# Kernel tuning notes

Hardware: AMD Instinct MI355X
Metric: run time of the kernel (lower is better)

Reference implementation:

```python
import jax, jax.numpy as jnp
import numpy as np

B, L, D, H, NS = 8, 1024, 64, 16, 3
DH = D // H          # head dim = 4 (scale = sqrt(4) = 2, matching K_.size(-1)**0.5)
DFF = 4 * D          # 256
EPS = 1e-5


def _bn(x_bld, gamma, beta):
    # BatchNorm1d in training mode on (B, C, L): normalize per-channel over (B, L)
    mean = jnp.mean(x_bld, axis=(0, 1))          # [D]
    var = jnp.mean((x_bld - mean) ** 2, axis=(0, 1))  # biased variance, as torch uses
    return gamma * (x_bld - mean) / jnp.sqrt(var + EPS) + beta


def setup_inputs() -> dict:
    key = jax.random.key(0)
    ks = jax.random.split(key, 12)
    s = 0.05
    inp = {
        "x": jax.random.normal(ks[0], (B, L, D), dtype=jnp.float32),
        # W_embed: Conv1d(64,64,k=1) == linear over channels
        "W_embed": jax.random.normal(ks[1], (D, D), dtype=jnp.float32) * s,
        "b_embed": jnp.zeros((D,), dtype=jnp.float32),
        "g0": jnp.ones((D,), dtype=jnp.float32),
        "be0": jnp.zeros((D,), dtype=jnp.float32),
        # shared attention weights (reused every stack)
        "Wq": jax.random.normal(ks[2], (D, D), dtype=jnp.float32) * s,
        "bq": jnp.zeros((D,), dtype=jnp.float32),
        "Wk": jax.random.normal(ks[3], (D, D), dtype=jnp.float32) * s,
        "bk": jnp.zeros((D,), dtype=jnp.float32),
        "Wv": jax.random.normal(ks[4], (D, D), dtype=jnp.float32) * s,
        "bv": jnp.zeros((D,), dtype=jnp.float32),
        "g_attn": jnp.ones((D,), dtype=jnp.float32),
        "be_attn": jnp.zeros((D,), dtype=jnp.float32),
        # shared feedforward (1x1 convs == channel linears)
        "W1": jax.random.normal(ks[5], (DFF, D), dtype=jnp.float32) * s,
        "b1": jnp.zeros((DFF,), dtype=jnp.float32),
        "W2": jax.random.normal(ks[6], (D, DFF), dtype=jnp.float32) * s,
        "b2": jnp.zeros((D,), dtype=jnp.float32),
        "g_ff": jnp.ones((D,), dtype=jnp.float32),
        "be_ff": jnp.zeros((D,), dtype=jnp.float32),
    }
    return inp


def reference(x, W_embed, b_embed, g0, be0, Wq, bq, Wk, bk, Wv, bv,
              g_attn, be_attn, W1, b1, W2, b2, g_ff, be_ff):
    # input embedding (1x1 conv) + batchnorm
    enc = x @ W_embed.T + b_embed              # [B, L, D]
    enc = _bn(enc, g0, be0)

    for _ in range(NS):  # num_stacks, SAME weights each stack (as in source)
        # --- multi-head attention (ReLU-activated QKV projections) ---
        Q = jax.nn.relu(enc @ Wq.T + bq)        # [B, L, D]
        K = jax.nn.relu(enc @ Wk.T + bk)
        V = jax.nn.relu(enc @ Wv.T + bv)
        q = Q.reshape(B, L, H, DH)
        k = K.reshape(B, L, H, DH)
        v = V.reshape(B, L, H, DH)
        scores = jnp.einsum('blhd,bmhd->bhlm', q, k) / jnp.sqrt(jnp.float32(DH))
        A = jax.nn.softmax(scores, axis=-1)     # [B, H, L, L]
        o = jnp.einsum('bhlm,bmhd->blhd', A, v).reshape(B, L, D)
        o = o + enc                             # residual
        enc = _bn(o, g_attn, be_attn)

        # --- feedforward: conv1d(k=1) -> ReLU -> conv1d(k=1) -> ReLU, residual, BN ---
        h = jax.nn.relu(enc @ W1.T + b1)        # [B, L, 4D]
        h = jax.nn.relu(h @ W2.T + b2)          # [B, L, D]
        h = h + enc                             # residual
        enc = _bn(h, g_ff, be_ff)
    return enc
```

## Files before the change

### kernel.cpp

```cpp
#include <hip/hip_runtime.h>
#include <math.h>

static constexpr int B_ = 8, L_ = 1024, D_ = 64, H_ = 16, DH_ = 4, DFF_ = 256;
static constexpr int M_ = B_ * L_;
static constexpr float EPS_ = 1e-5f;
static constexpr float INV_N_ = 1.0f / (float)M_;
static constexpr int PSTR_ = 512;

typedef _Float16 half4_ __attribute__((ext_vector_type(4)));
typedef __fp16   fp16x2 __attribute__((ext_vector_type(2)));
typedef float    f32x4  __attribute__((ext_vector_type(4)));

__global__ __launch_bounds__(256) void embed_kernel(
    const float* __restrict__ x, const float* __restrict__ W_embed,
    const float* __restrict__ wq, const float* __restrict__ wk,
    const float* __restrict__ wv, const float* __restrict__ w1,
    const float* __restrict__ w2, const float* __restrict__ bias,
    float* __restrict__ C, float* __restrict__ outParts,
    _Float16* __restrict__ wdst)
{
    const int t = threadIdx.x;
    {
        int base = (blockIdx.x * 256 + t) * 2;
        #pragma unroll
        for (int i = 0; i < 2; ++i) {
            int e = base + i;
            if (e < 45056) {
                float v;
                if      (e <  4096) v = wq[e];
                else if (e <  8192) v = wk[e - 4096];
                else if (e < 12288) v = wv[e - 8192];
                else if (e < 28672) v = w1[e - 12288];
                else                v = w2[e - 28672];
                wdst[e] = (_Float16)v;
            }
        }
    }

    __shared__ half4_ Alds[64][17];
    __shared__ half4_ Wlds[64][17];
    __shared__ float  wstats[4][128];
    const int m0 = blockIdx.x * 64;

    #pragma unroll
    for (int i = 0; i < 4; ++i) {
        int l = i * 256 + t;
        int row = l >> 4, c4 = l & 15;
        float4 av = *(const float4*)&x[(size_t)(m0 + row) * 64 + c4 * 4];
        Alds[row][c4] = half4_{(_Float16)av.x, (_Float16)av.y,
                               (_Float16)av.z, (_Float16)av.w};
        float4 wv4 = *(const float4*)&W_embed[(size_t)row * 64 + c4 * 4];
        Wlds[row][c4] = half4_{(_Float16)wv4.x, (_Float16)wv4.y,
                               (_Float16)wv4.z, (_Float16)wv4.w};
    }
    __syncthreads();

    const int lane = t & 63, w = t >> 6, g = lane >> 4, ml = lane & 15;

    f32x4 acc[4] = {};
    #pragma unroll
    for (int kci = 0; kci < 4; ++kci) {
        half4_ af = Alds[w * 16 + ml][kci * 4 + g];
        #pragma unroll
        for (int nt = 0; nt < 4; ++nt) {
            half4_ wf = Wlds[nt * 16 + ml][kci * 4 + g];
            acc[nt] = __builtin_amdgcn_mfma_f32_16x16x16f16(wf, af, acc[nt], 0, 0, 0);
        }
    }

    const int m = m0 + w * 16 + ml;
    float sv[4][4], qv[4][4];
    #pragma unroll
    for (int nt = 0; nt < 4; ++nt) {
        const int nc = nt * 16 + 4 * g;
        float4 bv4 = *(const float4*)&bias[nc];
        float r0 = acc[nt][0] + bv4.x, r1 = acc[nt][1] + bv4.y;
        float r2 = acc[nt][2] + bv4.z, r3 = acc[nt][3] + bv4.w;
        float4 o4 = { r0, r1, r2, r3 };
        *(float4*)&C[(size_t)m * 64 + nc] = o4;
        sv[nt][0] = r0; sv[nt][1] = r1; sv[nt][2] = r2; sv[nt][3] = r3;
        qv[nt][0] = r0 * r0; qv[nt][1] = r1 * r1;
        qv[nt][2] = r2 * r2; qv[nt][3] = r3 * r3;
    }

    #pragma unroll
    for (int d = 1; d <= 8; d <<= 1)
        #pragma unroll
        for (int nt = 0; nt < 4; ++nt)
            #pragma unroll
            for (int r = 0; r < 4; ++r) {
                sv[nt][r] += __shfl_xor(sv[nt][r], d);
                qv[nt][r] += __shfl_xor(qv[nt][r], d);
            }
    if (ml == 0) {
        #pragma unroll
        for (int nt = 0; nt < 4; ++nt)
            #pragma unroll
            for (int r = 0; r < 4; ++r) {
                int ch = nt * 16 + 4 * g + r;
                wstats[w][ch]      = sv[nt][r];
                wstats[w][64 + ch] = qv[nt][r];
            }
    }
    __syncthreads();
    if (t < 128) {
        float a = wstats[0][t] + wstats[1][t] + wstats[2][t] + wstats[3][t];
        outParts[(size_t)t * PSTR_ + blockIdx.x] = a;
    }
}

template<int NPB>
__global__ __launch_bounds__(256) void qkv_kernel(
    const float* __restrict__ tmpA,
    const _Float16* __restrict__ wqh, const float* __restrict__ bq,
    const _Float16* __restrict__ wkh, const float* __restrict__ bk,
    const _Float16* __restrict__ wvh, const float* __restrict__ bv,
    _Float16* __restrict__ qh, _Float16* __restrict__ kh, _Float16* __restrict__ vh,
    const float* __restrict__ partsIn,
    const float* __restrict__ gg, const float* __restrict__ bb)
{
    __shared__ half4_ Alds[64][17];
    __shared__ half4_ Wlds[64][17];
    __shared__ float  raw[128];
    __shared__ float  bnsc[64], bnsh[64];
    const int t    = threadIdx.x;
    const int m0   = blockIdx.x * 64;
    const int mode = blockIdx.y;

    const _Float16* W = (mode == 0) ? wqh : (mode == 1) ? wkh : wvh;
    const float* bias = (mode == 0) ? bq  : (mode == 1) ? bk  : bv;
    const float  sc2  = (mode == 0) ? 0.5f * 1.44269504088896340736f : 1.f;

    if (t < 128) {
        const float* pr = partsIn + (size_t)t * PSTR_;
        float a = 0.f;
        #pragma unroll
        for (int j = 0; j < NPB; j += 4) {
            float4 v4 = *(const float4*)&pr[j];
            a += v4.x + v4.y + v4.z + v4.w;
        }
        raw[t] = a;
    }
    __syncthreads();
    if (t < 64) {
        float mean = raw[t] * INV_N_;
        float ex2  = raw[64 + t] * INV_N_;
        float rs   = rsqrtf(ex2 - mean * mean + EPS_);
        float s2   = gg[t] * rs;
        bnsc[t] = s2;
        bnsh[t] = bb[t] - mean * s2;
    }
    __syncthreads();

    #pragma unroll
    for (int i = 0; i < 4; ++i) {
        int l = i * 256 + t;
        int row = l >> 4, c4 = l & 15;
        float4 av = *(const float4*)&tmpA[(size_t)(m0 + row) * 64 + c4 * 4];
        int c = c4 * 4;
        av.x = fmaf(av.x, bnsc[c + 0], bnsh[c + 0]);
        av.y = fmaf(av.y, bnsc[c + 1], bnsh[c + 1]);
        av.z = fmaf(av.z, bnsc[c + 2], bnsh[c + 2]);
        av.w = fmaf(av.w, bnsc[c + 3], bnsh[c + 3]);
        Alds[row][c4] = half4_{(_Float16)av.x, (_Float16)av.y,
                               (_Float16)av.z, (_Float16)av.w};
        Wlds[row][c4] = *(const half4_*)&W[(size_t)row * 64 + c4 * 4];
    }
    __syncthreads();

    const int lane = t & 63, w = t >> 6, g = lane >> 4, ml = lane & 15;

    f32x4 acc[4] = {};
    #pragma unroll
    for (int kci = 0; kci < 4; ++kci) {
        half4_ af = Alds[w * 16 + ml][kci * 4 + g];
        #pragma unroll
        for (int nt = 0; nt < 4; ++nt) {
            half4_ wf = Wlds[nt * 16 + ml][kci * 4 + g];
            acc[nt] = __builtin_amdgcn_mfma_f32_16x16x16f16(wf, af, acc[nt], 0, 0, 0);
        }
    }

    const int m    = m0 + w * 16 + ml;
    const int bidx = m >> 10, row = m & 1023;
    #pragma unroll
    for (int nt = 0; nt < 4; ++nt) {
        const int nc = nt * 16 + 4 * g;
        const int h  = nc >> 2;
        float4 bv4 = *(const float4*)&bias[nc];
        float r0 = fmaxf(acc[nt][0] + bv4.x, 0.f) * sc2;
        float r1 = fmaxf(acc[nt][1] + bv4.y, 0.f) * sc2;
        float r2 = fmaxf(acc[nt][2] + bv4.z, 0.f) * sc2;
        float r3 = fmaxf(acc[nt][3] + bv4.w, 0.f) * sc2;
        if (mode == 2) {
            size_t base = ((size_t)(bidx * 16 + h) * 4) * 1024 + row;
            vh[base + 0]    = (_Float16)r0;
            vh[base + 1024] = (_Float16)r1;
            vh[base + 2048] = (_Float16)r2;
            vh[base + 3072] = (_Float16)r3;
        } else {
            _Float16* Cq = (mode == 0) ? qh : kh;
            half4_ hs = { (_Float16)r0, (_Float16)r1, (_Float16)r2, (_Float16)r3 };
            *(half4_*)&Cq[((size_t)(bidx * 16 + h) * 1024 + row) * 4] = hs;
        }
    }
}

__global__ __launch_bounds__(256) void ffused_kernel(
    const float* __restrict__ tmpB, const _Float16* __restrict__ w1h,
    const float* __restrict__ b1, const _Float16* __restrict__ w2h,
    const float* __restrict__ b2, float* __restrict__ tmpA,
    const float* __restrict__ partsB,
    const float* __restrict__ gg, const float* __restrict__ bb,
    float* __restrict__ outParts)
{
    __shared__ half4_   Alds[16][17];
    __shared__ _Float16 H[16][264];
    __shared__ float    raw[128];
    __shared__ float    bnsc[64], bnsh[64];
    const int t  = threadIdx.x;
    const int m0 = blockIdx.x * 16;

    if (t < 128) {
        const float* pr = partsB + (size_t)t * PSTR_;
        float a = 0.f;
        #pragma unroll
        for (int j = 0; j < 64; j += 4) {
            float4 v4 = *(const float4*)&pr[j];
            a += v4.x + v4.y + v4.z + v4.w;
        }
        raw[t] = a;
    }
    __syncthreads();
    if (t < 64) {
        float mean = raw[t] * INV_N_;
        float ex2  = raw[64 + t] * INV_N_;
        float rs   = rsqrtf(ex2 - mean * mean + EPS_);
        float s2   = gg[t] * rs;
        bnsc[t] = s2;
        bnsh[t] = bb[t] - mean * s2;
    }
    __syncthreads();

    {
        int row = t >> 4, c4 = t & 15;
        float4 av = *(const float4*)&tmpB[(size_t)(m0 + row) * 64 + c4 * 4];
        int c = c4 * 4;
        av.x = fmaf(av.x, bnsc[c + 0], bnsh[c + 0]);
        av.y = fmaf(av.y, bnsc[c + 1], bnsh[c + 1]);
        av.z = fmaf(av.z, bnsc[c + 2], bnsh[c + 2]);
        av.w = fmaf(av.w, bnsc[c + 3], bnsh[c + 3]);
        Alds[row][c4] = half4_{(_Float16)av.x, (_Float16)av.y,
                               (_Float16)av.z, (_Float16)av.w};
    }
    __syncthreads();

    const int lane = t & 63, w = t >> 6, g = lane >> 4, ml = lane & 15;

    f32x4 acc1[4] = {};
    #pragma unroll
    for (int kci = 0; kci < 4; ++kci) {
        half4_ af = Alds[ml][kci * 4 + g];
        #pragma unroll
        for (int ntl = 0; ntl < 4; ++ntl) {
            int nt = w * 4 + ntl;
            half4_ wf = *(const half4_*)&w1h[(size_t)(nt * 16 + ml) * 64 + kci * 16 + 4 * g];
            acc1[ntl] = __builtin_amdgcn_mfma_f32_16x16x16f16(wf, af, acc1[ntl], 0, 0, 0);
        }
    }
    #pragma unroll
    for (int ntl = 0; ntl < 4; ++ntl) {
        int nt = w * 4 + ntl;
        float4 b1v = *(const float4*)&b1[nt * 16 + 4 * g];
        half4_ hv = { (_Float16)fmaxf(acc1[ntl][0] + b1v.x, 0.f),
                      (_Float16)fmaxf(acc1[ntl][1] + b1v.y, 0.f),
                      (_Float16)fmaxf(acc1[ntl][2] + b1v.z, 0.f),
                      (_Float16)fmaxf(acc1[ntl][3] + b1v.w, 0.f) };
        *(half4_*)&H[ml][nt * 16 + 4 * g] = hv;
    }
    __syncthreads();

    f32x4 acc2 = {};
    #pragma unroll
    for (int kci2 = 0; kci2 < 16; ++kci2) {
        half4_ af2 = *(const half4_*)&H[ml][kci2 * 16 + 4 * g];
        half4_ wf2 = *(const half4_*)&w2h[(size_t)(w * 16 + ml) * 256 + kci2 * 16 + 4 * g];
        acc2 = __builtin_amdgcn_mfma_f32_16x16x16f16(wf2, af2, acc2, 0, 0, 0);
    }

    const int m  = m0 + ml;
    const int nc = w * 16 + 4 * g;
    float4 b2v = *(const float4*)&b2[nc];
    half4_ rr  = Alds[ml][w * 4 + g];
    float r0 = fmaxf(acc2[0] + b2v.x, 0.f) + (float)rr[0];
    float r1 = fmaxf(acc2[1] + b2v.y, 0.f) + (float)rr[1];
    float r2 = fmaxf(acc2[2] + b2v.z, 0.f) + (float)rr[2];
    float r3 = fmaxf(acc2[3] + b2v.w, 0.f) + (float)rr[3];
    float4 o4 = { r0, r1, r2, r3 };
    *(float4*)&tmpA[(size_t)m * 64 + nc] = o4;

    float sv[4] = { r0, r1, r2, r3 };
    float qv[4] = { r0 * r0, r1 * r1, r2 * r2, r3 * r3 };
    #pragma unroll
    for (int d = 1; d <= 8; d <<= 1)
        #pragma unroll
        for (int r = 0; r < 4; ++r) {
            sv[r] += __shfl_xor(sv[r], d);
            qv[r] += __shfl_xor(qv[r], d);
        }
    if (ml == 0) {
        #pragma unroll
        for (int r = 0; r < 4; ++r) {
            outParts[(size_t)(nc + r) * PSTR_ + blockIdx.x]      = sv[r];
            outParts[(size_t)(64 + nc + r) * PSTR_ + blockIdx.x] = qv[r];
        }
    }
}

template<int NPB>
__global__ __launch_bounds__(256) void attn_kernel(
    const _Float16* __restrict__ q, const _Float16* __restrict__ k,
    const _Float16* __restrict__ v, const float* __restrict__ encRaw,
    float* __restrict__ out, const float* __restrict__ partsIn,
    const float* __restrict__ gPrev, const float* __restrict__ bPrev,
    float* __restrict__ partsOut)
{
    __shared__ uint2 klds[1024];
    __shared__ uint2 vlds[1024];
    __shared__ float raw8[8], rsc[4], rsh[4];
    __shared__ float wred[4][8];

    const int bid = blockIdx.x;
    const int qc  = bid & 7;
    const int h   = (bid >> 3) & 15;
    const int b   = bid >> 7;
    const int t   = threadIdx.x;

    if (t < 8) {
        const int row = (t >> 2) * 64 + 4 * h + (t & 3);
        const float* pr = partsIn + (size_t)row * PSTR_;
        float a = 0.f;
        #pragma unroll
        for (int j = 0; j < NPB; j += 4) {
            float4 v4 = *(const float4*)&pr[j];
            a += v4.x + v4.y + v4.z + v4.w;
        }
        raw8[t] = a;
    }
    if (t < 4) {
        float mean = raw8[t] * INV_N_;
        float ex2  = raw8[4 + t] * INV_N_;
        float rs   = rsqrtf(ex2 - mean * mean + EPS_);
        float s2   = gPrev[4 * h + t] * rs;
        rsc[t] = s2;
        rsh[t] = bPrev[4 * h + t] - mean * s2;
    }

    const size_t baseqk = (size_t)(b * 16 + h) * 4096;

    #pragma unroll
    for (int i = 0; i < 4; ++i) {
        int key = i * 256 + t;
        klds[key] = *(const uint2*)&k[baseqk + (size_t)key * 4];
        int e = (t >> 2) * 16 + (t & 3) * 4 + i;
        vlds[e] = *(const uint2*)&v[baseqk + (size_t)i * 1024 + t * 4];
    }
    __syncthreads();

    const int lane = t & 63;
    const int wv2  = t >> 6;
    const int ln16 = lane & 15;
    const int g16  = lane >> 4;
    const int q0   = qc * 128 + wv2 * 32;

    half4_ qf0 = { 0, 0, 0, 0 }, qf1 = { 0, 0, 0, 0 };
    if (lane < 16) {
        qf0 = __builtin_bit_cast(half4_,
              *(const uint2*)&q[baseqk + (size_t)(q0 + ln16) * 4]);
        qf1 = __builtin_bit_cast(half4_,
              *(const uint2*)&q[baseqk + (size_t)(q0 + 16 + ln16) * 4]);
    }

    const half4_ ones = { (_Float16)1.f, (_Float16)1.f, (_Float16)1.f, (_Float16)1.f };
    const f32x4  fz   = { 0.f, 0.f, 0.f, 0.f };
    f32x4 o0 = fz, o1 = fz;

    #pragma unroll 4
    for (int c = 0; c < 64; ++c) {
        half4_ ka = __builtin_bit_cast(half4_, klds[c * 16 + ln16]);
        half4_ va = __builtin_bit_cast(half4_, vlds[c * 16 + g16 * 4 + (ln16 & 3)]);
        if (ln16 == 4) va = ones;

        f32x4 s0 = __builtin_amdgcn_mfma_f32_16x16x16f16(ka, qf0, fz, 0, 0, 0);
        f32x4 s1 = __builtin_amdgcn_mfma_f32_16x16x16f16(ka, qf1, fz, 0, 0, 0);

        float e00 = __builtin_amdgcn_exp2f(s0[0]);
        float e01 = __builtin_amdgcn_exp2f(s0[1]);
        float e02 = __builtin_amdgcn_exp2f(s0[2]);
        float e03 = __builtin_amdgcn_exp2f(s0[3]);
        float e10 = __builtin_amdgcn_exp2f(s1[0]);
        float e11 = __builtin_amdgcn_exp2f(s1[1]);
        float e12 = __builtin_amdgcn_exp2f(s1[2]);
        float e13 = __builtin_amdgcn_exp2f(s1[3]);

        fp16x2 a0 = __builtin_amdgcn_cvt_pkrtz(e00, e01);
        fp16x2 b0 = __builtin_amdgcn_cvt_pkrtz(e02, e03);
        fp16x2 a1 = __builtin_amdgcn_cvt_pkrtz(e10, e11);
        fp16x2 b1 = __builtin_amdgcn_cvt_pkrtz(e12, e13);
        half4_ p0 = __builtin_bit_cast(half4_, __builtin_shufflevector(a0, b0, 0, 1, 2, 3));
        half4_ p1 = __builtin_bit_cast(half4_, __builtin_shufflevector(a1, b1, 0, 1, 2, 3));

        o0 = __builtin_amdgcn_mfma_f32_16x16x16f16(va, p0, o0, 0, 0, 0);
        o1 = __builtin_amdgcn_mfma_f32_16x16x16f16(va, p1, o1, 0, 0, 0);
    }

    float ls0 = __shfl(o0[0], 16 + ln16);
    float ls1 = __shfl(o1[0], 16 + ln16);

    float4 r0v = { 0.f, 0.f, 0.f, 0.f }, r1v = r0v;
    if (lane < 16) {
        {
            const size_t gi = (size_t)(b * L_ + q0 + ln16) * D_ + h * DH_;
            const float inv = 1.0f / ls0;
            const float4 e4 = *(const float4*)&encRaw[gi];
            r0v.x = fmaf(o0[0], inv, fmaf(e4.x, rsc[0], rsh[0]));
            r0v.y = fmaf(o0[1], inv, fmaf(e4.y, rsc[1], rsh[1]));
            r0v.z = fmaf(o0[2], inv, fmaf(e4.z, rsc[2], rsh[2]));
            r0v.w = fmaf(o0[3], inv, fmaf(e4.w, rsc[3], rsh[3]));
            *(float4*)&out[gi] = r0v;
        }
        {
            const size_t gi = (size_t)(b * L_ + q0 + 16 + ln16) * D_ + h * DH_;
            const float inv = 1.0f / ls1;
            const float4 e4 = *(const float4*)&encRaw[gi];
            r1v.x = fmaf(o1[0], inv, fmaf(e4.x, rsc[0], rsh[0]));
            r1v.y = fmaf(o1[1], inv, fmaf(e4.y, rsc[1], rsh[1]));
            r1v.z = fmaf(o1[2], inv, fmaf(e4.z, rsc[2], rsh[2]));
            r1v.w = fmaf(o1[3], inv, fmaf(e4.w, rsc[3], rsh[3]));
            *(float4*)&out[gi] = r1v;
        }
    }

    float s4[4] = { r0v.x + r1v.x, r0v.y + r1v.y, r0v.z + r1v.z, r0v.w + r1v.w };
    float q4[4] = { r0v.x*r0v.x + r1v.x*r1v.x, r0v.y*r0v.y + r1v.y*r1v.y,
                    r0v.z*r0v.z + r1v.z*r1v.z, r0v.w*r0v.w + r1v.w*r1v.w };
    #pragma unroll
    for (int d2 = 1; d2 <= 8; d2 <<= 1) {
        #pragma unroll
        for (int j = 0; j < 4; ++j) {
            s4[j] += __shfl_xor(s4[j], d2);
            q4[j] += __shfl_xor(q4[j], d2);
        }
    }
    if (lane == 0) {
        #pragma unroll
        for (int j = 0; j < 4; ++j) { wred[wv2][j] = s4[j]; wred[wv2][4 + j] = q4[j]; }
    }
    __syncthreads();
    if (t < 8) {
        float a = wred[0][t] + wred[1][t] + wred[2][t] + wred[3][t];
        const int row = (t >> 2) * 64 + 4 * h + (t & 3);
        partsOut[(size_t)row * PSTR_ + (b * 8 + qc)] = a;
    }
}

__global__ __launch_bounds__(256) void bn_apply_kernel(
    const float* __restrict__ x, const float* __restrict__ parts,
    const float* __restrict__ gamma, const float* __restrict__ beta,
    float* __restrict__ y)
{
    __shared__ float fstats[128];
    const int t = threadIdx.x;
    if (t < 128) {
        const float* pr = parts + (size_t)t * PSTR_;
        float a = 0.f;
        #pragma unroll
        for (int j = 0; j < 512; j += 4) {
            float4 v4 = *(const float4*)&pr[j];
            a += v4.x + v4.y + v4.z + v4.w;
        }
        fstats[t] = a;
    }
    __syncthreads();

    const int idx = blockIdx.x * 256 + t;
    const int c = (idx & 15) << 2;
    float4 xv = ((const float4*)x)[idx];
    float4 sm = *(const float4*)&fstats[c];
    float4 sq = *(const float4*)&fstats[64 + c];
    float4 g  = *(const float4*)&gamma[c];
    float4 be = *(const float4*)&beta[c];

    float mean[4] = {sm.x * INV_N_, sm.y * INV_N_, sm.z * INV_N_, sm.w * INV_N_};
    float ex2[4]  = {sq.x * INV_N_, sq.y * INV_N_, sq.z * INV_N_, sq.w * INV_N_};
    float xa[4] = {xv.x, xv.y, xv.z, xv.w};
    float ga[4] = {g.x, g.y, g.z, g.w};
    float ba[4] = {be.x, be.y, be.z, be.w};
    float ya[4];
    #pragma unroll
    for (int i = 0; i < 4; ++i) {
        float var = ex2[i] - mean[i] * mean[i];
        float rs = rsqrtf(var + EPS_);
        ya[i] = ga[i] * (xa[i] - mean[i]) * rs + ba[i];
    }
    float4 r = {ya[0], ya[1], ya[2], ya[3]};
    ((float4*)y)[idx] = r;
}

extern "C" void kernel_launch(void* const* d_in, const int* in_sizes, int n_in,
                              void* d_out, int out_size, void* d_ws, size_t ws_size,
                              hipStream_t stream)
{
    const float* x       = (const float*)d_in[0];
    const float* W_embed = (const float*)d_in[1];
    const float* b_embed = (const float*)d_in[2];
    const float* g0      = (const float*)d_in[3];
    const float* be0     = (const float*)d_in[4];
    const float* Wq      = (const float*)d_in[5];
    const float* bq      = (const float*)d_in[6];
    const float* Wk      = (const float*)d_in[7];
    const float* bk      = (const float*)d_in[8];
    const float* Wv      = (const float*)d_in[9];
    const float* bv      = (const float*)d_in[10];
    const float* g_attn  = (const float*)d_in[11];
    const float* be_attn = (const float*)d_in[12];
    const float* W1      = (const float*)d_in[13];
    const float* b1      = (const float*)d_in[14];
    const float* W2      = (const float*)d_in[15];
    const float* b2      = (const float*)d_in[16];
    const float* g_ff    = (const float*)d_in[17];
    const float* be_ff   = (const float*)d_in[18];

    float* ws     = (float*)d_ws;
    float* tmpA   = ws;
    float* tmpB   = ws + 524288;
    float* partsA = ws + 1048576;
    float* partsB = ws + 1114112;
    _Float16* hb  = (_Float16*)(ws + 1179648);
    _Float16* qh  = hb;
    _Float16* kh  = hb + 524288;
    _Float16* vh  = hb + 1048576;
    _Float16* wqh = hb + 1572864;
    _Float16* wkh = wqh + 4096;
    _Float16* wvh = wkh + 4096;
    _Float16* w1h = wvh + 4096;
    _Float16* w2h = w1h + 16384;
    float* out = (float*)d_out;

    const dim3 blk(256);

    embed_kernel<<<128, blk, 0, stream>>>(
        x, W_embed, Wq, Wk, Wv, W1, W2, b_embed, tmpA, partsA, wqh);

    for (int s = 0; s < 3; ++s) {
        const float* gP  = (s == 0) ? g0  : g_ff;
        const float* beP = (s == 0) ? be0 : be_ff;
        if (s == 0) {
            qkv_kernel<128><<<dim3(128, 3), blk, 0, stream>>>(
                tmpA, wqh, bq, wkh, bk, wvh, bv, qh, kh, vh, partsA, gP, beP);
            attn_kernel<128><<<1024, blk, 0, stream>>>(
                qh, kh, vh, tmpA, tmpB, partsA, gP, beP, partsB);
        } else {
            qkv_kernel<512><<<dim3(128, 3), blk, 0, stream>>>(
                tmpA, wqh, bq, wkh, bk, wvh, bv, qh, kh, vh, partsA, gP, beP);
            attn_kernel<512><<<1024, blk, 0, stream>>>(
                qh, kh, vh, tmpA, tmpB, partsA, gP, beP, partsB);
        }
        ffused_kernel<<<512, blk, 0, stream>>>(
            tmpB, w1h, b1, w2h, b2, tmpA, partsB, g_attn, be_attn, partsA);
    }
    bn_apply_kernel<<<512, blk, 0, stream>>>(tmpA, partsA, g_ff, be_ff, out);
}
```

Measured before the change: 192.4 us.

## Merge all stages into one cooperative persistent kernel with grid syncs

Result: faster. 172.4 us (-10.4%).

```diff
diff --git a/kernel.cpp b/kernel.cpp
--- a/kernel.cpp
+++ b/kernel.cpp
@@ -1,57 +1,47 @@
 #include <hip/hip_runtime.h>
+#include <hip/hip_cooperative_groups.h>
 #include <math.h>
+
+namespace cg = cooperative_groups;
 
 static constexpr int B_ = 8, L_ = 1024, D_ = 64, H_ = 16, DH_ = 4, DFF_ = 256;
 static constexpr int M_ = B_ * L_;
 static constexpr float EPS_ = 1e-5f;
 static constexpr float INV_N_ = 1.0f / (float)M_;
-static constexpr int PSTR_ = 512;
+static constexpr int PSTR_ = 256;
+static constexpr unsigned SMEM_ = 32768;
 
 typedef _Float16 half4_ __attribute__((ext_vector_type(4)));
 typedef __fp16   fp16x2 __attribute__((ext_vector_type(2)));
 typedef float    f32x4  __attribute__((ext_vector_type(4)));
 
-__global__ __launch_bounds__(256) void embed_kernel(
-    const float* __restrict__ x, const float* __restrict__ W_embed,
-    const float* __restrict__ wq, const float* __restrict__ wk,
-    const float* __restrict__ wv, const float* __restrict__ w1,
-    const float* __restrict__ w2, const float* __restrict__ bias,
-    float* __restrict__ C, float* __restrict__ outParts,
-    _Float16* __restrict__ wdst)
-{
-    const int t = threadIdx.x;
-    {
-        int base = (blockIdx.x * 256 + t) * 2;
-        #pragma unroll
-        for (int i = 0; i < 2; ++i) {
-            int e = base + i;
-            if (e < 45056) {
-                float v;
-                if      (e <  4096) v = wq[e];
-                else if (e <  8192) v = wk[e - 4096];
-                else if (e < 12288) v = wv[e - 8192];
-                else if (e < 28672) v = w1[e - 12288];
-                else                v = w2[e - 28672];
-                wdst[e] = (_Float16)v;
-            }
-        }
-    }
-
-    __shared__ half4_ Alds[64][17];
-    __shared__ half4_ Wlds[64][17];
-    __shared__ float  wstats[4][128];
-    const int m0 = blockIdx.x * 64;
+struct MParams {
+    const float *x, *W_embed, *b_embed, *g0, *be0;
+    const float *Wq, *bq, *Wk, *bk, *Wv, *bv, *g_attn, *be_attn;
+    const float *W1, *b1, *W2, *b2, *g_ff, *be_ff;
+    float *tmpA, *tmpB, *partsA, *partsB;
+    _Float16 *qh, *kh, *vh, *h1, *wqh, *wkh, *wvh, *w1h, *w2h;
+    float *out;
+};
+
+__device__ __forceinline__ void embed_work(char* sm, int blk, const MParams& p)
+{
+    half4_* Alds  = (half4_*)sm;
+    half4_* Wlds  = (half4_*)(sm + 8704);
+    float*  wstat = (float*)(sm + 17408);
+    const int t  = threadIdx.x;
+    const int m0 = blk * 64;
 
     #pragma unroll
     for (int i = 0; i < 4; ++i) {
         int l = i * 256 + t;
         int row = l >> 4, c4 = l & 15;
-        float4 av = *(const float4*)&x[(size_t)(m0 + row) * 64 + c4 * 4];
-        Alds[row][c4] = half4_{(_Float16)av.x, (_Float16)av.y,
-                               (_Float16)av.z, (_Float16)av.w};
-        float4 wv4 = *(const float4*)&W_embed[(size_t)row * 64 + c4 * 4];
-        Wlds[row][c4] = half4_{(_Float16)wv4.x, (_Float16)wv4.y,
-                               (_Float16)wv4.z, (_Float16)wv4.w};
+        float4 av = *(const float4*)&p.x[(size_t)(m0 + row) * 64 + c4 * 4];
+        Alds[row * 17 + c4] = half4_{(_Float16)av.x, (_Float16)av.y,
+                                     (_Float16)av.z, (_Float16)av.w};
+        float4 wv4 = *(const float4*)&p.W_embed[(size_t)row * 64 + c4 * 4];
+        Wlds[row * 17 + c4] = half4_{(_Float16)wv4.x, (_Float16)wv4.y,
+                                     (_Float16)wv4.z, (_Float16)wv4.w};
     }
     __syncthreads();
 
@@ -60,10 +50,10 @@
     f32x4 acc[4] = {};
     #pragma unroll
     for (int kci = 0; kci < 4; ++kci) {
-        half4_ af = Alds[w * 16 + ml][kci * 4 + g];
+        half4_ af = Alds[(w * 16 + ml) * 17 + kci * 4 + g];
         #pragma unroll
         for (int nt = 0; nt < 4; ++nt) {
-            half4_ wf = Wlds[nt * 16 + ml][kci * 4 + g];
+            half4_ wf = Wlds[(nt * 16 + ml) * 17 + kci * 4 + g];
             acc[nt] = __builtin_amdgcn_mfma_f32_16x16x16f16(wf, af, acc[nt], 0, 0, 0);
         }
     }
@@ -73,11 +63,11 @@
     #pragma unroll
     for (int nt = 0; nt < 4; ++nt) {
         const int nc = nt * 16 + 4 * g;
-        float4 bv4 = *(const float4*)&bias[nc];
+        float4 bv4 = *(const float4*)&p.b_embed[nc];
         float r0 = acc[nt][0] + bv4.x, r1 = acc[nt][1] + bv4.y;
         float r2 = acc[nt][2] + bv4.z, r3 = acc[nt][3] + bv4.w;
         float4 o4 = { r0, r1, r2, r3 };
-        *(float4*)&C[(size_t)m * 64 + nc] = o4;
+        *(float4*)&p.tmpA[(size_t)m * 64 + nc] = o4;
         sv[nt][0] = r0; sv[nt][1] = r1; sv[nt][2] = r2; sv[nt][3] = r3;
         qv[nt][0] = r0 * r0; qv[nt][1] = r1 * r1;
         qv[nt][2] = r2 * r2; qv[nt][3] = r3 * r3;
@@ -98,41 +88,50 @@
             #pragma unroll
             for (int r = 0; r < 4; ++r) {
                 int ch = nt * 16 + 4 * g + r;
-                wstats[w][ch]      = sv[nt][r];
-                wstats[w][64 + ch] = qv[nt][r];
+                wstat[w * 128 + ch]      = sv[nt][r];
+                wstat[w * 128 + 64 + ch] = qv[nt][r];
             }
     }
     __syncthreads();
     if (t < 128) {
-        float a = wstats[0][t] + wstats[1][t] + wstats[2][t] + wstats[3][t];
-        outParts[(size_t)t * PSTR_ + blockIdx.x] = a;
+        float a = wstat[t] + wstat[128 + t] + wstat[256 + t] + wstat[384 + t];
+        p.partsA[(size_t)t * PSTR_ + blk] = a;
+    }
+}
+
+__device__ __forceinline__ void wcvt_work(int blk, int t, const MParams& p)
+{
+    int e = (blk - 128) * 256 + t;
+    if (e < 45056) {
+        float v;
+        if      (e <  4096) v = p.Wq[e];
+        else if (e <  8192) v = p.Wk[e - 4096];
+        else if (e < 12288) v = p.Wv[e - 8192];
+        else if (e < 28672) v = p.W1[e - 12288];
+        else                v = p.W2[e - 28672];
+        p.wqh[e] = (_Float16)v;
     }
 }
 
 template<int NPB>
-__global__ __launch_bounds__(256) void qkv_kernel(
-    const float* __restrict__ tmpA,
-    const _Float16* __restrict__ wqh, const float* __restrict__ bq,
-    const _Float16* __restrict__ wkh, const float* __restrict__ bk,
-    const _Float16* __restrict__ wvh, const float* __restrict__ bv,
-    _Float16* __restrict__ qh, _Float16* __restrict__ kh, _Float16* __restrict__ vh,
-    const float* __restrict__ partsIn,
-    const float* __restrict__ gg, const float* __restrict__ bb)
-{
-    __shared__ half4_ Alds[64][17];
-    __shared__ half4_ Wlds[64][17];
-    __shared__ float  raw[128];
-    __shared__ float  bnsc[64], bnsh[64];
+__device__ __forceinline__ void qkv_work(char* sm, int blk, const MParams& p,
+                                         const float* gg, const float* bb)
+{
+    half4_* Alds = (half4_*)sm;
+    half4_* Wlds = (half4_*)(sm + 8704);
+    float*  raw  = (float*)(sm + 17408);
+    float*  bnsc = (float*)(sm + 17920);
+    float*  bnsh = (float*)(sm + 18176);
     const int t    = threadIdx.x;
-    const int m0   = blockIdx.x * 64;
-    const int mode = blockIdx.y;
-
-    const _Float16* W = (mode == 0) ? wqh : (mode == 1) ? wkh : wvh;
-    const float* bias = (mode == 0) ? bq  : (mode == 1) ? bk  : bv;
+    const int m0   = (blk & 127) * 64;
+    const int mode = blk >> 7;
+
+    const _Float16* W = (mode == 0) ? p.wqh : (mode == 1) ? p.wkh : p.wvh;
+    const float* bias = (mode == 0) ? p.bq  : (mode == 1) ? p.bk  : p.bv;
     const float  sc2  = (mode == 0) ? 0.5f * 1.44269504088896340736f : 1.f;
 
     if (t < 128) {
-        const float* pr = partsIn + (size_t)t * PSTR_;
+        const float* pr = p.partsA + (size_t)t * PSTR_;
         float a = 0.f;
         #pragma unroll
         for (int j = 0; j < NPB; j += 4) {
@@ -156,15 +155,15 @@
     for (int i = 0; i < 4; ++i) {
         int l = i * 256 + t;
         int row = l >> 4, c4 = l & 15;
-        float4 av = *(const float4*)&tmpA[(size_t)(m0 + row) * 64 + c4 * 4];
+        float4 av = *(const float4*)&p.tmpA[(size_t)(m0 + row) * 64 + c4 * 4];
         int c = c4 * 4;
         av.x = fmaf(av.x, bnsc[c + 0], bnsh[c + 0]);
         av.y = fmaf(av.y, bnsc[c + 1], bnsh[c + 1]);
         av.z = fmaf(av.z, bnsc[c + 2], bnsh[c + 2]);
         av.w = fmaf(av.w, bnsc[c + 3], bnsh[c + 3]);
-        Alds[row][c4] = half4_{(_Float16)av.x, (_Float16)av.y,
-                               (_Float16)av.z, (_Float16)av.w};
-        Wlds[row][c4] = *(const half4_*)&W[(size_t)row * 64 + c4 * 4];
+        Alds[row * 17 + c4] = half4_{(_Float16)av.x, (_Float16)av.y,
+                                     (_Float16)av.z, (_Float16)av.w};
+        Wlds[row * 17 + c4] = *(const half4_*)&W[(size_t)row * 64 + c4 * 4];
     }
     __syncthreads();
 
@@ -173,10 +172,10 @@
     f32x4 acc[4] = {};
     #pragma unroll
     for (int kci = 0; kci < 4; ++kci) {
-        half4_ af = Alds[w * 16 + ml][kci * 4 + g];
+        half4_ af = Alds[(w * 16 + ml) * 17 + kci * 4 + g];
         #pragma unroll
         for (int nt = 0; nt < 4; ++nt) {
-            half4_ wf = Wlds[nt * 16 + ml][kci * 4 + g];
+            half4_ wf = Wlds[(nt * 16 + ml) * 17 + kci * 4 + g];
             acc[nt] = __builtin_amdgcn_mfma_f32_16x16x16f16(wf, af, acc[nt], 0, 0, 0);
         }
     }
@@ -194,151 +193,37 @@
         float r3 = fmaxf(acc[nt][3] + bv4.w, 0.f) * sc2;
         if (mode == 2) {
             size_t base = ((size_t)(bidx * 16 + h) * 4) * 1024 + row;
-            vh[base + 0]    = (_Float16)r0;
-            vh[base + 1024] = (_Float16)r1;
-            vh[base + 2048] = (_Float16)r2;
-            vh[base + 3072] = (_Float16)r3;
+            p.vh[base + 0]    = (_Float16)r0;
+            p.vh[base + 1024] = (_Float16)r1;
+            p.vh[base + 2048] = (_Float16)r2;
+            p.vh[base + 3072] = (_Float16)r3;
         } else {
-            _Float16* Cq = (mode == 0) ? qh : kh;
+            _Float16* Cq = (mode == 0) ? p.qh : p.kh;
             half4_ hs = { (_Float16)r0, (_Float16)r1, (_Float16)r2, (_Float16)r3 };
             *(half4_*)&Cq[((size_t)(bidx * 16 + h) * 1024 + row) * 4] = hs;
         }
     }
 }
 
-__global__ __launch_bounds__(256) void ffused_kernel(
-    const float* __restrict__ tmpB, const _Float16* __restrict__ w1h,
-    const float* __restrict__ b1, const _Float16* __restrict__ w2h,
-    const float* __restrict__ b2, float* __restrict__ tmpA,
-    const float* __restrict__ partsB,
-    const float* __restrict__ gg, const float* __restrict__ bb,
-    float* __restrict__ outParts)
-{
-    __shared__ half4_   Alds[16][17];
-    __shared__ _Float16 H[16][264];
-    __shared__ float    raw[128];
-    __shared__ float    bnsc[64], bnsh[64];
+template<int NPB>
+__device__ __forceinline__ void attn_work(char* sm, int unit, const MParams& p,
+                                          const float* gPrev, const float* bPrev)
+{
+    uint2* klds = (uint2*)sm;
+    uint2* vlds = (uint2*)(sm + 8192);
+    float* raw8 = (float*)(sm + 16384);
+    float* rsc  = (float*)(sm + 16416);
+    float* rsh  = (float*)(sm + 16432);
+    float* wred = (float*)(sm + 16448);
+
+    const int qc = unit & 7;
+    const int h  = (unit >> 3) & 15;
+    const int b  = unit >> 7;
     const int t  = threadIdx.x;
-    const int m0 = blockIdx.x * 16;
-
-    if (t < 128) {
-        const float* pr = partsB + (size_t)t * PSTR_;
-        float a = 0.f;
-        #pragma unroll
-        for (int j = 0; j < 64; j += 4) {
-            float4 v4 = *(const float4*)&pr[j];
-            a += v4.x + v4.y + v4.z + v4.w;
-        }
-        raw[t] = a;
-    }
-    __syncthreads();
-    if (t < 64) {
-        float mean = raw[t] * INV_N_;
-        float ex2  = raw[64 + t] * INV_N_;
-        float rs   = rsqrtf(ex2 - mean * mean + EPS_);
-        float s2   = gg[t] * rs;
-        bnsc[t] = s2;
-        bnsh[t] = bb[t] - mean * s2;
-    }
-    __syncthreads();
-
-    {
-        int row = t >> 4, c4 = t & 15;
-        float4 av = *(const float4*)&tmpB[(size_t)(m0 + row) * 64 + c4 * 4];
-        int c = c4 * 4;
-        av.x = fmaf(av.x, bnsc[c + 0], bnsh[c + 0]);
-        av.y = fmaf(av.y, bnsc[c + 1], bnsh[c + 1]);
-        av.z = fmaf(av.z, bnsc[c + 2], bnsh[c + 2]);
-        av.w = fmaf(av.w, bnsc[c + 3], bnsh[c + 3]);
-        Alds[row][c4] = half4_{(_Float16)av.x, (_Float16)av.y,
-                               (_Float16)av.z, (_Float16)av.w};
-    }
-    __syncthreads();
-
-    const int lane = t & 63, w = t >> 6, g = lane >> 4, ml = lane & 15;
-
-    f32x4 acc1[4] = {};
-    #pragma unroll
-    for (int kci = 0; kci < 4; ++kci) {
-        half4_ af = Alds[ml][kci * 4 + g];
-        #pragma unroll
-        for (int ntl = 0; ntl < 4; ++ntl) {
-            int nt = w * 4 + ntl;
-            half4_ wf = *(const half4_*)&w1h[(size_t)(nt * 16 + ml) * 64 + kci * 16 + 4 * g];
-            acc1[ntl] = __builtin_amdgcn_mfma_f32_16x16x16f16(wf, af, acc1[ntl], 0, 0, 0);
-        }
-    }
-    #pragma unroll
-    for (int ntl = 0; ntl < 4; ++ntl) {
-        int nt = w * 4 + ntl;
-        float4 b1v = *(const float4*)&b1[nt * 16 + 4 * g];
-        half4_ hv = { (_Float16)fmaxf(acc1[ntl][0] + b1v.x, 0.f),
-                      (_Float16)fmaxf(acc1[ntl][1] + b1v.y, 0.f),
-                      (_Float16)fmaxf(acc1[ntl][2] + b1v.z, 0.f),
-                      (_Float16)fmaxf(acc1[ntl][3] + b1v.w, 0.f) };
-        *(half4_*)&H[ml][nt * 16 + 4 * g] = hv;
-    }
-    __syncthreads();
-
-    f32x4 acc2 = {};
-    #pragma unroll
-    for (int kci2 = 0; kci2 < 16; ++kci2) {
-        half4_ af2 = *(const half4_*)&H[ml][kci2 * 16 + 4 * g];
-        half4_ wf2 = *(const half4_*)&w2h[(size_t)(w * 16 + ml) * 256 + kci2 * 16 + 4 * g];
-        acc2 = __builtin_amdgcn_mfma_f32_16x16x16f16(wf2, af2, acc2, 0, 0, 0);
-    }
-
-    const int m  = m0 + ml;
-    const int nc = w * 16 + 4 * g;
-    float4 b2v = *(const float4*)&b2[nc];
-    half4_ rr  = Alds[ml][w * 4 + g];
-    float r0 = fmaxf(acc2[0] + b2v.x, 0.f) + (float)rr[0];
-    float r1 = fmaxf(acc2[1] + b2v.y, 0.f) + (float)rr[1];
-    float r2 = fmaxf(acc2[2] + b2v.z, 0.f) + (float)rr[2];
-    float r3 = fmaxf(acc2[3] + b2v.w, 0.f) + (float)rr[3];
-    float4 o4 = { r0, r1, r2, r3 };
-    *(float4*)&tmpA[(size_t)m * 64 + nc] = o4;
-
-    float sv[4] = { r0, r1, r2, r3 };
-    float qv[4] = { r0 * r0, r1 * r1, r2 * r2, r3 * r3 };
-    #pragma unroll
-    for (int d = 1; d <= 8; d <<= 1)
-        #pragma unroll
-        for (int r = 0; r < 4; ++r) {
-            sv[r] += __shfl_xor(sv[r], d);
-            qv[r] += __shfl_xor(qv[r], d);
-        }
-    if (ml == 0) {
-        #pragma unroll
-        for (int r = 0; r < 4; ++r) {
-            outParts[(size_t)(nc + r) * PSTR_ + blockIdx.x]      = sv[r];
-            outParts[(size_t)(64 + nc + r) * PSTR_ + blockIdx.x] = qv[r];
-        }
-    }
-}
-
-template<int NPB>
-__global__ __launch_bounds__(256) void attn_kernel(
-    const _Float16* __restrict__ q, const _Float16* __restrict__ k,
-    const _Float16* __restrict__ v, const float* __restrict__ encRaw,
-    float* __restrict__ out, const float* __restrict__ partsIn,
-    const float* __restrict__ gPrev, const float* __restrict__ bPrev,
-    float* __restrict__ partsOut)
-{
-    __shared__ uint2 klds[1024];
-    __shared__ uint2 vlds[1024];
-    __shared__ float raw8[8], rsc[4], rsh[4];
-    __shared__ float wred[4][8];
-
-    const int bid = blockIdx.x;
-    const int qc  = bid & 7;
-    const int h   = (bid >> 3) & 15;
-    const int b   = bid >> 7;
-    const int t   = threadIdx.x;
 
     if (t < 8) {
         const int row = (t >> 2) * 64 + 4 * h + (t & 3);
-        const float* pr = partsIn + (size_t)row * PSTR_;
+        const float* pr = p.partsA + (size_t)row * PSTR_;
         float a = 0.f;
         #pragma unroll
         for (int j = 0; j < NPB; j += 4) {
@@ -361,9 +246,9 @@
     #pragma unroll
     for (int i = 0; i < 4; ++i) {
         int key = i * 256 + t;
-        klds[key] = *(const uint2*)&k[baseqk + (size_t)key * 4];
+        klds[key] = *(const uint2*)&p.kh[baseqk + (size_t)key * 4];
         int e = (t >> 2) * 16 + (t & 3) * 4 + i;
-        vlds[e] = *(const uint2*)&v[baseqk + (size_t)i * 1024 + t * 4];
+        vlds[e] = *(const uint2*)&p.vh[baseqk + (size_t)i * 1024 + t * 4];
     }
     __syncthreads();
 
@@ -376,9 +261,9 @@
     half4_ qf0 = { 0, 0, 0, 0 }, qf1 = { 0, 0, 0, 0 };
     if (lane < 16) {
         qf0 = __builtin_bit_cast(half4_,
-              *(const uint2*)&q[baseqk + (size_t)(q0 + ln16) * 4]);
+              *(const uint2*)&p.qh[baseqk + (size_t)(q0 + ln16) * 4]);
         qf1 = __builtin_bit_cast(half4_,
-              *(const uint2*)&q[baseqk + (size_t)(q0 + 16 + ln16) * 4]);
+              *(const uint2*)&p.qh[baseqk + (size_t)(q0 + 16 + ln16) * 4]);
     }
 
     const half4_ ones = { (_Float16)1.f, (_Float16)1.f, (_Float16)1.f, (_Float16)1.f };
@@ -422,22 +307,22 @@
         {
             const size_t gi = (size_t)(b * L_ + q0 + ln16) * D_ + h * DH_;
             const float inv = 1.0f / ls0;
-            const float4 e4 = *(const float4*)&encRaw[gi];
+            const float4 e4 = *(const float4*)&p.tmpA[gi];
             r0v.x = fmaf(o0[0], inv, fmaf(e4.x, rsc[0], rsh[0]));
             r0v.y = fmaf(o0[1], inv, fmaf(e4.y, rsc[1], rsh[1]));
             r0v.z = fmaf(o0[2], inv, fmaf(e4.z, rsc[2], rsh[2]));
             r0v.w = fmaf(o0[3], inv, fmaf(e4.w, rsc[3], rsh[3]));
-            *(float4*)&out[gi] = r0v;
+            *(float4*)&p.tmpB[gi] = r0v;
         }
         {
             const size_t gi = (size_t)(b * L_ + q0 + 16 + ln16) * D_ + h * DH_;
             const float inv = 1.0f / ls1;
-            const float4 e4 = *(const float4*)&encRaw[gi];
+            const float4 e4 = *(const float4*)&p.tmpA[gi];
             r1v.x = fmaf(o1[0], inv, fmaf(e4.x, rsc[0], rsh[0]));
             r1v.y = fmaf(o1[1], inv, fmaf(e4.y, rsc[1], rsh[1]));
             r1v.z = fmaf(o1[2], inv, fmaf(e4.z, rsc[2], rsh[2]));
             r1v.w = fmaf(o1[3], inv, fmaf(e4.w, rsc[3], rsh[3]));
-            *(float4*)&out[gi] = r1v;
+            *(float4*)&p.tmpB[gi] = r1v;
         }
     }
 
@@ -454,28 +339,196 @@
     }
     if (lane == 0) {
         #pragma unroll
-        for (int j = 0; j < 4; ++j) { wred[wv2][j] = s4[j]; wred[wv2][4 + j] = q4[j]; }
+        for (int j = 0; j < 4; ++j) { wred[wv2 * 8 + j] = s4[j]; wred[wv2 * 8 + 4 + j] = q4[j]; }
     }
     __syncthreads();
     if (t < 8) {
-        float a = wred[0][t] + wred[1][t] + wred[2][t] + wred[3][t];
+        float a = wred[t] + wred[8 + t] + wred[16 + t] + wred[24 + t];
         const int row = (t >> 2) * 64 + 4 * h + (t & 3);
-        partsOut[(size_t)row * PSTR_ + (b * 8 + qc)] = a;
-    }
-}
-
-__global__ __launch_bounds__(256) void bn_apply_kernel(
-    const float* __restrict__ x, const float* __restrict__ parts,
-    const float* __restrict__ gamma, const float* __restrict__ beta,
-    float* __restrict__ y)
-{
-    __shared__ float fstats[128];
+        p.partsB[(size_t)row * PSTR_ + (b * 8 + qc)] = a;
+    }
+}
+
+__device__ __forceinline__ void ff1_work(char* sm, int blk, const MParams& p)
+{
+    half4_* Alds = (half4_*)sm;
+    half4_* Wlds = (half4_*)(sm + 8704);
+    float*  raw  = (float*)(sm + 17408);
+    float*  bnsc = (float*)(sm + 17920);
+    float*  bnsh = (float*)(sm + 18176);
+    const int t  = threadIdx.x;
+    const int m0 = (blk & 127) * 64;
+    const int n0 = (blk >> 7) * 64;
+
+    if (t < 128) {
+        const float* pr = p.partsB + (size_t)t * PSTR_;
+        float a = 0.f;
+        #pragma unroll
+        for (int j = 0; j < 64; j += 4) {
+            float4 v4 = *(const float4*)&pr[j];
+            a += v4.x + v4.y + v4.z + v4.w;
+        }
+        raw[t] = a;
+    }
+    __syncthreads();
+    if (t < 64) {
+        float mean = raw[t] * INV_N_;
+        float ex2  = raw[64 + t] * INV_N_;
+        float rs   = rsqrtf(ex2 - mean * mean + EPS_);
+        float s2   = p.g_attn[t] * rs;
+        bnsc[t] = s2;
+        bnsh[t] = p.be_attn[t] - mean * s2;
+    }
+    __syncthreads();
+
+    #pragma unroll
+    for (int i = 0; i < 4; ++i) {
+        int l = i * 256 + t;
+        int row = l >> 4, c4 = l & 15;
+        float4 av = *(const float4*)&p.tmpB[(size_t)(m0 + row) * 64 + c4 * 4];
+        int c = c4 * 4;
+        av.x = fmaf(av.x, bnsc[c + 0], bnsh[c + 0]);
+        av.y = fmaf(av.y, bnsc[c + 1], bnsh[c + 1]);
+        av.z = fmaf(av.z, bnsc[c + 2], bnsh[c + 2]);
+        av.w = fmaf(av.w, bnsc[c + 3], bnsh[c + 3]);
+        Alds[row * 17 + c4] = half4_{(_Float16)av.x, (_Float16)av.y,
+                                     (_Float16)av.z, (_Float16)av.w};
+        Wlds[row * 17 + c4] = *(const half4_*)&p.w1h[(size_t)(n0 + row) * 64 + c4 * 4];
+    }
+    __syncthreads();
+
+    const int lane = t & 63, w = t >> 6, g = lane >> 4, ml = lane & 15;
+
+    f32x4 acc[4] = {};
+    #pragma unroll
+    for (int kci = 0; kci < 4; ++kci) {
+        half4_ af = Alds[(w * 16 + ml) * 17 + kci * 4 + g];
+        #pragma unroll
+        for (int nt = 0; nt < 4; ++nt) {
+            half4_ wf = Wlds[(nt * 16 + ml) * 17 + kci * 4 + g];
+            acc[nt] = __builtin_amdgcn_mfma_f32_16x16x16f16(wf, af, acc[nt], 0, 0, 0);
+        }
+    }
+
+    const int m = m0 + w * 16 + ml;
+    #pragma unroll
+    for (int nt = 0; nt < 4; ++nt) {
+        const int nc = n0 + nt * 16 + 4 * g;
+        float4 bv4 = *(const float4*)&p.b1[nc];
+        half4_ hs = { (_Float16)fmaxf(acc[nt][0] + bv4.x, 0.f),
+                      (_Float16)fmaxf(acc[nt][1] + bv4.y, 0.f),
+                      (_Float16)fmaxf(acc[nt][2] + bv4.z, 0.f),
+                      (_Float16)fmaxf(acc[nt][3] + bv4.w, 0.f) };
+        *(half4_*)&p.h1[(size_t)m * 256 + nc] = hs;
+    }
+}
+
+__device__ __forceinline__ void ff2_work(char* sm, int blk, const MParams& p)
+{
+    const int t  = threadIdx.x;
+    const int mb = blk & 255;
+    const int nh = blk >> 8;
+    const int m0 = mb * 32;
+    const int lane = t & 63, w = t >> 6, g = lane >> 4, ml = lane & 15;
+    const int mhalf = w & 1, ntile = w >> 1;
+    const int ch = nh * 32 + ntile * 16 + 4 * g;
+
+    float* scratch = (float*)sm;
+    if (t < 128) {
+        const float* pr = p.partsB + (size_t)t * PSTR_;
+        float a = 0.f;
+        #pragma unroll
+        for (int j = 0; j < 64; j += 4) {
+            float4 v4 = *(const float4*)&pr[j];
+            a += v4.x + v4.y + v4.z + v4.w;
+        }
+        scratch[t] = a;
+    }
+    __syncthreads();
+    float scR[4], shR[4];
+    #pragma unroll
+    for (int i = 0; i < 4; ++i) {
+        float mean = scratch[ch + i] * INV_N_;
+        float ex2  = scratch[64 + ch + i] * INV_N_;
+        float rs   = rsqrtf(ex2 - mean * mean + EPS_);
+        float s2   = p.g_attn[ch + i] * rs;
+        scR[i] = s2;
+        shR[i] = p.be_attn[ch + i] - mean * s2;
+    }
+    __syncthreads();
+
+    half4_* Alds = (half4_*)sm;
+    half4_* Wlds = (half4_*)(sm + 16384);
+    #pragma unroll
+    for (int i = 0; i < 8; ++i) {
+        int l = i * 256 + t;
+        int row = l >> 6, c4 = l & 63;
+        int sw = c4 ^ (row & 7);
+        Alds[row * 64 + sw] = *(const half4_*)&p.h1[(size_t)(m0 + row) * 256 + c4 * 4];
+        Wlds[row * 64 + sw] = *(const half4_*)&p.w2h[(size_t)(nh * 32 + row) * 256 + c4 * 4];
+    }
+    __syncthreads();
+
+    f32x4 acc = {};
+    const int arow = mhalf * 16 + ml, wrow = ntile * 16 + ml;
+    #pragma unroll
+    for (int kci = 0; kci < 16; ++kci) {
+        half4_ af = Alds[arow * 64 + ((kci * 4 + g) ^ (arow & 7))];
+        half4_ wf = Wlds[wrow * 64 + ((kci * 4 + g) ^ (wrow & 7))];
+        acc = __builtin_amdgcn_mfma_f32_16x16x16f16(wf, af, acc, 0, 0, 0);
+    }
+
+    const int m = m0 + mhalf * 16 + ml;
+    float4 b2v = *(const float4*)&p.b2[ch];
+    float r0 = fmaxf(acc[0] + b2v.x, 0.f);
+    float r1 = fmaxf(acc[1] + b2v.y, 0.f);
+    float r2 = fmaxf(acc[2] + b2v.z, 0.f);
+    float r3 = fmaxf(acc[3] + b2v.w, 0.f);
+    float4 rv = *(const float4*)&p.tmpB[(size_t)m * 64 + ch];
+    r0 += fmaf(rv.x, scR[0], shR[0]);
+    r1 += fmaf(rv.y, scR[1], shR[1]);
+    r2 += fmaf(rv.z, scR[2], shR[2]);
+    r3 += fmaf(rv.w, scR[3], shR[3]);
+    float4 o4 = { r0, r1, r2, r3 };
+    *(float4*)&p.tmpA[(size_t)m * 64 + ch] = o4;
+
+    float sv[4] = { r0, r1, r2, r3 };
+    float qv[4] = { r0 * r0, r1 * r1, r2 * r2, r3 * r3 };
+    #pragma unroll
+    for (int d = 1; d <= 8; d <<= 1)
+        #pragma unroll
+        for (int r = 0; r < 4; ++r) {
+            sv[r] += __shfl_xor(sv[r], d);
+            qv[r] += __shfl_xor(qv[r], d);
+        }
+    __syncthreads();
+    float* wstat = (float*)sm;
+    if (ml == 0) {
+        #pragma unroll
+        for (int r = 0; r < 4; ++r) {
+            wstat[w * 32 + 4 * g + r]      = sv[r];
+            wstat[w * 32 + 16 + 4 * g + r] = qv[r];
+        }
+    }
+    __syncthreads();
+    if (t < 64) {
+        const int nt2 = t >> 5, j = t & 31;
+        float a = wstat[(nt2 * 2 + 0) * 32 + j] + wstat[(nt2 * 2 + 1) * 32 + j];
+        const int chL = j & 15, isSq = j >> 4;
+        const int row = isSq * 64 + nh * 32 + nt2 * 16 + chL;
+        p.partsA[(size_t)row * PSTR_ + mb] = a;
+    }
+}
+
+__device__ __forceinline__ void bn_work(char* sm, int blk, const MParams& p)
+{
+    float* fstats = (float*)sm;
     const int t = threadIdx.x;
     if (t < 128) {
-        const float* pr = parts + (size_t)t * PSTR_;
+        const float* pr = p.partsA + (size_t)t * PSTR_;
         float a = 0.f;
         #pragma unroll
-        for (int j = 0; j < 512; j += 4) {
+        for (int j = 0; j < 256; j += 4) {
             float4 v4 = *(const float4*)&pr[j];
             a += v4.x + v4.y + v4.z + v4.w;
         }
@@ -483,19 +536,19 @@
     }
     __syncthreads();
 
-    const int idx = blockIdx.x * 256 + t;
+    const int idx = blk * 256 + t;
     const int c = (idx & 15) << 2;
-    float4 xv = ((const float4*)x)[idx];
-    float4 sm = *(const float4*)&fstats[c];
-    float4 sq = *(const float4*)&fstats[64 + c];
-    float4 g  = *(const float4*)&gamma[c];
-    float4 be = *(const float4*)&beta[c];
-
-    float mean[4] = {sm.x * INV_N_, sm.y * INV_N_, sm.z * INV_N_, sm.w * INV_N_};
+    float4 xv = ((const float4*)p.tmpA)[idx];
+    float4 sm4 = *(const float4*)&fstats[c];
+    float4 sq  = *(const float4*)&fstats[64 + c];
+    float4 g4  = *(const float4*)&p.g_ff[c];
+    float4 be4 = *(const float4*)&p.be_ff[c];
+
+    float mean[4] = {sm4.x * INV_N_, sm4.y * INV_N_, sm4.z * INV_N_, sm4.w * INV_N_};
     float ex2[4]  = {sq.x * INV_N_, sq.y * INV_N_, sq.z * INV_N_, sq.w * INV_N_};
     float xa[4] = {xv.x, xv.y, xv.z, xv.w};
-    float ga[4] = {g.x, g.y, g.z, g.w};
-    float ba[4] = {be.x, be.y, be.z, be.w};
+    float ga[4] = {g4.x, g4.y, g4.z, g4.w};
+    float ba[4] = {be4.x, be4.y, be4.z, be4.w};
     float ya[4];
     #pragma unroll
     for (int i = 0; i < 4; ++i) {
@@ -504,70 +557,144 @@
         ya[i] = ga[i] * (xa[i] - mean[i]) * rs + ba[i];
     }
     float4 r = {ya[0], ya[1], ya[2], ya[3]};
-    ((float4*)y)[idx] = r;
+    ((float4*)p.out)[idx] = r;
+}
+
+__global__ void __launch_bounds__(256, 2) mega_kernel(MParams p)
+{
+    extern __shared__ char sm[];
+    cg::grid_group grid = cg::this_grid();
+    const int blk = blockIdx.x;
+    const int t   = threadIdx.x;
+
+    if (blk < 128)      embed_work(sm, blk, p);
+    else if (blk < 304) wcvt_work(blk, t, p);
+    grid.sync();
+
+    #pragma unroll 1
+    for (int s = 0; s < 3; ++s) {
+        const float* gP  = (s == 0) ? p.g0  : p.g_ff;
+        const float* beP = (s == 0) ? p.be0 : p.be_ff;
+        if (blk < 384) {
+            if (s == 0) qkv_work<128>(sm, blk, p, gP, beP);
+            else        qkv_work<256>(sm, blk, p, gP, beP);
+        }
+        grid.sync();
+        if (s == 0) { attn_work<128>(sm, blk, p, gP, beP);
+                      attn_work<128>(sm, blk + 512, p, gP, beP); }
+        else        { attn_work<256>(sm, blk, p, gP, beP);
+                      attn_work<256>(sm, blk + 512, p, gP, beP); }
+        grid.sync();
+        ff1_work(sm, blk, p);
+        grid.sync();
+        ff2_work(sm, blk, p);
+        grid.sync();
+    }
+    bn_work(sm, blk, p);
+}
+
+__global__ void __launch_bounds__(256) fb_phase0(MParams p)
+{
+    extern __shared__ char sm[];
+    if (blockIdx.x < 128) embed_work(sm, blockIdx.x, p);
+    else                  wcvt_work(blockIdx.x, threadIdx.x, p);
+}
+template<int NPB>
+__global__ void __launch_bounds__(256) fb_qkv(MParams p, const float* gg, const float* bb)
+{
+    extern __shared__ char sm[];
+    qkv_work<NPB>(sm, blockIdx.x, p, gg, bb);
+}
+template<int NPB>
+__global__ void __launch_bounds__(256) fb_attn(MParams p, const float* gg, const float* bb)
+{
+    extern __shared__ char sm[];
+    attn_work<NPB>(sm, blockIdx.x, p, gg, bb);
+}
+__global__ void __launch_bounds__(256) fb_ff1(MParams p)
+{
+    extern __shared__ char sm[];
+    ff1_work(sm, blockIdx.x, p);
+}
+__global__ void __launch_bounds__(256) fb_ff2(MParams p)
+{
+    extern __shared__ char sm[];
+    ff2_work(sm, blockIdx.x, p);
+}
+__global__ void __launch_bounds__(256) fb_bn(MParams p)
+{
+    extern __shared__ char sm[];
+    bn_work(sm, blockIdx.x, p);
 }
 
 extern "C" void kernel_launch(void* const* d_in, const int* in_sizes, int n_in,
                               void* d_out, int out_size, void* d_ws, size_t ws_size,
                               hipStream_t stream)
 {
-    const float* x       = (const float*)d_in[0];
-    const float* W_embed = (const float*)d_in[1];
-    const float* b_embed = (const float*)d_in[2];
-    const float* g0      = (const float*)d_in[3];
-    const float* be0     = (const float*)d_in[4];
-    const float* Wq      = (const float*)d_in[5];
-    const float* bq      = (const float*)d_in[6];
-    const float* Wk      = (const float*)d_in[7];
-    const float* bk      = (const float*)d_in[8];
-    const float* Wv      = (const float*)d_in[9];
-    const float* bv      = (const float*)d_in[10];
-    const float* g_attn  = (const float*)d_in[11];
-    const float* be_attn = (const float*)d_in[12];
-    const float* W1      = (const float*)d_in[13];
-    const float* b1      = (const float*)d_in[14];
-    const float* W2      = (const float*)d_in[15];
-    const float* b2      = (const float*)d_in[16];
-    const float* g_ff    = (const float*)d_in[17];
-    const float* be_ff   = (const float*)d_in[18];
-
-    float* ws     = (float*)d_ws;
-    float* tmpA   = ws;
-    float* tmpB   = ws + 524288;
-    float* partsA = ws + 1048576;
-    float* partsB = ws + 1114112;
-    _Float16* hb  = (_Float16*)(ws + 1179648);
-    _Float16* qh  = hb;
-    _Float16* kh  = hb + 524288;
-    _Float16* vh  = hb + 1048576;
-    _Float16* wqh = hb + 1572864;
-    _Float16* wkh = wqh + 4096;
-    _Float16* wvh = wkh + 4096;
-    _Float16* w1h = wvh + 4096;
-    _Float16* w2h = w1h + 16384;
-    float* out = (float*)d_out;
+    MParams p;
+    p.x       = (const float*)d_in[0];
+    p.W_embed = (const float*)d_in[1];
+    p.b_embed = (const float*)d_in[2];
+    p.g0      = (const float*)d_in[3];
+    p.be0     = (const float*)d_in[4];
+    p.Wq      = (const float*)d_in[5];
+    p.bq      = (const float*)d_in[6];
+    p.Wk      = (const float*)d_in[7];
+    p.bk      = (const float*)d_in[8];
+    p.Wv      = (const float*)d_in[9];
+    p.bv      = (const float*)d_in[10];
+    p.g_attn  = (const float*)d_in[11];
+    p.be_attn = (const float*)d_in[12];
+    p.W1      = (const float*)d_in[13];
+    p.b1      = (const float*)d_in[14];
+    p.W2      = (const float*)d_in[15];
+    p.b2      = (const float*)d_in[16];
+    p.g_ff    = (const float*)d_in[17];
+    p.be_ff   = (const float*)d_in[18];
+
+    float* ws = (float*)d_ws;
+    p.tmpA   = ws;
+    p.tmpB   = ws + 524288;
+    p.partsA = ws + 1048576;
+    p.partsB = ws + 1081344;
+    _Float16* hb = (_Float16*)(ws + 1114112);
+    p.qh  = hb;
+    p.kh  = hb + 524288;
+    p.vh  = hb + 1048576;
+    p.h1  = hb + 1572864;
+    p.wqh = hb + 3670016;
+    p.wkh = p.wqh + 4096;
+    p.wvh = p.wkh + 4096;
+    p.w1h = p.wvh + 4096;
+    p.w2h = p.w1h + 16384;
+    p.out = (float*)d_out;
+
+    int nb = 0;
+    hipError_t qerr = hipOccupancyMaxActiveBlocksPerMultiprocessor(
+        &nb, (const void*)mega_kernel, 256, SMEM_);
+    bool done = false;
+    if (qerr == hipSuccess && nb >= 2) {
+        void* args[] = { &p };
+        hipError_t e = hipLaunchCooperativeKernel(
+            (const void*)mega_kernel, dim3(512), dim3(256), args, SMEM_, stream);
+        done = (e == hipSuccess);
+    }
+    if (done) return;
 
     const dim3 blk(256);
-
-    embed_kernel<<<128, blk, 0, stream>>>(
-        x, W_embed, Wq, Wk, Wv, W1, W2, b_embed, tmpA, partsA, wqh);
-
+    fb_phase0<<<304, blk, 19456, stream>>>(p);
     for (int s = 0; s < 3; ++s) {
-        const float* gP  = (s == 0) ? g0  : g_ff;
-        const float* beP = (s == 0) ? be0 : be_ff;
+        const float* gP  = (s == 0) ? p.g0  : p.g_ff;
+        const float* beP = (s == 0) ? p.be0 : p.be_ff;
         if (s == 0) {
-            qkv_kernel<128><<<dim3(128, 3), blk, 0, stream>>>(
-                tmpA, wqh, bq, wkh, bk, wvh, bv, qh, kh, vh, partsA, gP, beP);
-            attn_kernel<128><<<1024, blk, 0, stream>>>(
-                qh, kh, vh, tmpA, tmpB, partsA, gP, beP, partsB);
+            fb_qkv<128><<<384, blk, 18432, stream>>>(p, gP, beP);
+            fb_attn<128><<<1024, blk, 16576, stream>>>(p, gP, beP);
         } else {
-            qkv_kernel<512><<<dim3(128, 3), blk, 0, stream>>>(
-                tmpA, wqh, bq, wkh, bk, wvh, bv, qh, kh, vh, partsA, gP, beP);
-            attn_kernel<512><<<1024, blk, 0, stream>>>(
-                qh, kh, vh, tmpA, tmpB, partsA, gP, beP, partsB);
-        }
-        ffused_kernel<<<512, blk, 0, stream>>>(
-            tmpB, w1h, b1, w2h, b2, tmpA, partsB, g_attn, be_attn, partsA);
-    }
-    bn_apply_kernel<<<512, blk, 0, stream>>>(tmpA, partsA, g_ff, be_ff, out);
-}
+            fb_qkv<256><<<384, blk, 18432, stream>>>(p, gP, beP);
+            fb_attn<256><<<1024, blk, 16576, stream>>>(p, gP, beP);
+        }
+        fb_ff1<<<512, blk, 18432, stream>>>(p);
+        fb_ff2<<<512, blk, 32768, stream>>>(p);
+    }
+    fb_bn<<<512, blk, 512, stream>>>(p);
+}
```
